# Kernel optimization log

Hardware: AMD Instinct MI355X
Metric: run time of the kernel (lower is better)

## Reference

```python
import jax, jax.numpy as jnp
import numpy as np

N_HEAD = 32
N_KV_HEAD = 8
HEAD_DIM = 64
N_EMBD = 2048
B, T = 2, 2048
ROPE_BASE = 10000.0


def _rope_cos_sin(T, head_dim, dtype):
    pos = jnp.arange(T, dtype=jnp.float32)
    dim_arr = jnp.arange(0, head_dim, 2, dtype=jnp.float32)
    freqs = ROPE_BASE ** (-dim_arr / head_dim)
    theta = jnp.outer(pos, freqs)                      # [T, hd/2]
    cos = jnp.concatenate([jnp.cos(theta), jnp.cos(theta)], axis=-1)  # [T, hd]
    sin = jnp.concatenate([jnp.sin(theta), jnp.sin(theta)], axis=-1)
    # broadcast to [1, T, 1, hd]
    return cos[None, :, None, :].astype(dtype), sin[None, :, None, :].astype(dtype)


def _rotate_half(v):
    h = v.shape[-1] // 2
    return jnp.concatenate([-v[..., h:], v[..., :h]], axis=-1)


def setup_inputs() -> dict:
    key = jax.random.key(0)
    kx, kq, kk, kv, ko = jax.random.split(key, 5)
    s = 1.0 / np.sqrt(N_EMBD)
    return {
        "x": jax.random.normal(kx, (B, T, N_EMBD), dtype=jnp.float32),
        "wq": jax.random.normal(kq, (N_EMBD, N_HEAD * HEAD_DIM), dtype=jnp.float32) * s,
        "wk": jax.random.normal(kk, (N_EMBD, N_KV_HEAD * HEAD_DIM), dtype=jnp.float32) * s,
        "wv": jax.random.normal(kv, (N_EMBD, N_KV_HEAD * HEAD_DIM), dtype=jnp.float32) * s,
        "wo": jax.random.normal(ko, (N_HEAD * HEAD_DIM, N_EMBD), dtype=jnp.float32) * s,
    }


def reference(x, wq, wk, wv, wo):
    Bx, Tx, C = x.shape
    n_rep = N_HEAD // N_KV_HEAD

    xq = (x @ wq).reshape(Bx, Tx, N_HEAD, HEAD_DIM)
    xk = (x @ wk).reshape(Bx, Tx, N_KV_HEAD, HEAD_DIM)
    xv = (x @ wv).reshape(Bx, Tx, N_KV_HEAD, HEAD_DIM)

    cos, sin = _rope_cos_sin(Tx, HEAD_DIM, x.dtype)
    xq = xq * cos + _rotate_half(xq) * sin
    xk = xk * cos + _rotate_half(xk) * sin

    # GQA: repeat_interleave KV heads to match query heads
    xk = jnp.repeat(xk, n_rep, axis=2)  # [B, T, H, hd]
    xv = jnp.repeat(xv, n_rep, axis=2)

    scale = 1.0 / np.sqrt(HEAD_DIM)
    # scores: [B, H, T, T]
    scores = jnp.einsum("bqhd,bkhd->bhqk", xq, xk) * scale
    causal = jnp.tril(jnp.ones((Tx, Tx), dtype=bool))
    scores = jnp.where(causal[None, None], scores, -jnp.inf)
    probs = jax.nn.softmax(scores, axis=-1)

    out = jnp.einsum("bhqk,bkhd->bqhd", probs, xv).reshape(Bx, Tx, N_HEAD * HEAD_DIM)
    return out @ wo
```

## Files before the change

kernel.cpp:

```cpp
#include <hip/hip_runtime.h>
#include <hip/hip_bf16.h>
#include <cstdint>
#include <cstddef>

#define B_ 2
#define T_ 2048
#define H_ 32
#define KVH_ 8
#define D_ 64
#define C_ 2048
#define NQKV 3072

typedef short short8 __attribute__((ext_vector_type(8)));
typedef float f32x4 __attribute__((ext_vector_type(4)));
typedef unsigned short u16;

__device__ __forceinline__ u16 f2b(float f) {
  union { float f; unsigned u; } x; x.f = f;
  unsigned r = x.u + 0x7fffu + ((x.u >> 16) & 1u);
  return (u16)(r >> 16);
}

__device__ __forceinline__ void gload16(const void* g, void* l) {
  __builtin_amdgcn_global_load_lds(
      (const __attribute__((address_space(1))) unsigned int*)g,
      (__attribute__((address_space(3))) unsigned int*)l,
      16, 0, 0);
}

__device__ __forceinline__ f32x4 mfma16(short8 a, short8 b, f32x4 c) {
  return __builtin_amdgcn_mfma_f32_16x16x32_bf16(a, b, c, 0, 0, 0);
}

__device__ __forceinline__ unsigned cvtpk(float lo_, float hi_) {
  unsigned r;
  asm("v_cvt_pk_bf16_f32 %0, %1, %2" : "=v"(r) : "v"(lo_), "v"(hi_));
  return r;
}

__global__ void k_tbl(float* __restrict__ tbl) {
  int i = blockIdx.x * 256 + threadIdx.x;
  int t = i >> 5, f = i & 31;
  double freq = pow(10000.0, -(double)f / 32.0);
  double th = (double)t * freq;
  tbl[i * 2 + 0] = (float)cos(th);
  tbl[i * 2 + 1] = (float)sin(th);
}

__global__ void k_cvtx(const float* __restrict__ x, u16* __restrict__ xb) {
  int i = blockIdx.x * 256 + threadIdx.x;
  float4 v = ((const float4*)x)[i];
  ushort4 o;
  o.x = f2b(v.x); o.y = f2b(v.y); o.z = f2b(v.z); o.w = f2b(v.w);
  ((ushort4*)xb)[i] = o;
}

__global__ void k_transw(const float* __restrict__ src, u16* __restrict__ dst, int N) {
  __shared__ float t[32][33];
  int tx = threadIdx.x, ty = threadIdx.y;
  int k0 = blockIdx.y * 32, n0 = blockIdx.x * 32;
#pragma unroll
  for (int i = 0; i < 4; i++)
    t[ty + i * 8][tx] = src[(size_t)(k0 + ty + i * 8) * N + n0 + tx];
  __syncthreads();
#pragma unroll
  for (int i = 0; i < 4; i++) {
    int nl = ty + i * 8;
    dst[(size_t)(n0 + nl) * 2048 + k0 + tx] = f2b(t[tx][nl]);
  }
}

__global__ __launch_bounds__(256, 2) void k_gemm(const u16* __restrict__ A,
                                                 const u16* __restrict__ Bt,
                                                 float* __restrict__ Cc,
                                                 int M, int N, int K) {
  __shared__ __align__(16) u16 As[128 * 32];
  __shared__ __align__(16) u16 Bs[128 * 32];
  const int tid = threadIdx.x;
  const int w = tid >> 6, l = tid & 63;
  const int lo = l & 15, hi = l >> 4;
  const int m0 = blockIdx.y * 128, n0 = blockIdx.x * 128;
  const int wr = w >> 1, wc = w & 1;
  f32x4 acc[4][4];
#pragma unroll
  for (int i = 0; i < 4; i++)
#pragma unroll
    for (int j = 0; j < 4; j++) acc[i][j] = (f32x4){0.f, 0.f, 0.f, 0.f};

  for (int k0 = 0; k0 < K; k0 += 32) {
#pragma unroll
    for (int i = 0; i < 2; i++) {
      int cid = i * 256 + tid;
      int row = cid >> 2, kc = cid & 3;
      gload16(A + (size_t)(m0 + row) * K + k0 + kc * 8, &As[(i * 256 + w * 64) * 8]);
      gload16(Bt + (size_t)(n0 + row) * K + k0 + kc * 8, &Bs[(i * 256 + w * 64) * 8]);
    }
    __syncthreads();
    short8 a[4], b[4];
#pragma unroll
    for (int i = 0; i < 4; i++)
      a[i] = *(const short8*)&As[(wr * 64 + i * 16 + lo) * 32 + hi * 8];
#pragma unroll
    for (int j = 0; j < 4; j++)
      b[j] = *(const short8*)&Bs[(wc * 64 + j * 16 + lo) * 32 + hi * 8];
#pragma unroll
    for (int i = 0; i < 4; i++)
#pragma unroll
      for (int j = 0; j < 4; j++) acc[i][j] = mfma16(a[i], b[j], acc[i][j]);
    __syncthreads();
  }
  const int r0 = m0 + wr * 64, c0 = n0 + wc * 64;
#pragma unroll
  for (int i = 0; i < 4; i++)
#pragma unroll
    for (int j = 0; j < 4; j++) {
      f32x4 v = acc[i][j];
      int col = c0 + j * 16 + lo;
      int rw = r0 + i * 16 + hi * 4;
#pragma unroll
      for (int r = 0; r < 4; r++) Cc[(size_t)(rw + r) * N + col] = v[r];
    }
}

__global__ void k_rope(const float* __restrict__ QKV, const float* __restrict__ tbl,
                       u16* __restrict__ Qb, u16* __restrict__ Kb, u16* __restrict__ Vb) {
  int bt = blockIdx.x;
  int b = bt >> 11, t = bt & 2047;
  const float* row = QKV + (size_t)bt * NQKV;
  const float2* cs = (const float2*)tbl + (size_t)t * 32;
  int tid = threadIdx.x;
  const float QS = 0.125f * 1.44269504089f;
#pragma unroll
  for (int i = 0; i < 4; i++) {
    int p = i * 256 + tid;
    int h = p >> 5, dd = p & 31;
    float2 c = cs[dd];
    float q0 = row[h * 64 + dd], q1 = row[h * 64 + dd + 32];
    float o0 = (q0 * c.x - q1 * c.y) * QS;
    float o1 = (q1 * c.x + q0 * c.y) * QS;
    size_t base = ((size_t)(b * H_ + h) * T_ + t) * 64 + dd;
    Qb[base] = f2b(o0);
    Qb[base + 32] = f2b(o1);
  }
  {
    int kvh = tid >> 5, dd = tid & 31;
    float2 c = cs[dd];
    float k0v = row[2048 + kvh * 64 + dd], k1v = row[2048 + kvh * 64 + dd + 32];
    size_t base = ((size_t)(b * KVH_ + kvh) * T_ + t) * 64 + dd;
    Kb[base] = f2b(k0v * c.x - k1v * c.y);
    Kb[base + 32] = f2b(k1v * c.x + k0v * c.y);
  }
#pragma unroll
  for (int i = 0; i < 2; i++) {
    int e = i * 256 + tid;
    int kvh = e >> 6, dd = e & 63;
    Vb[((size_t)(b * KVH_ + kvh) * T_ + t) * 64 + dd] = f2b(row[2560 + e]);
  }
}

__global__ void k_vtrans(const u16* __restrict__ Vb, u16* __restrict__ Vt) {
  __shared__ u16 tl[64][65];
  int bk = blockIdx.y;
  int t0 = blockIdx.x * 64;
  int tid = threadIdx.x;
#pragma unroll
  for (int i = 0; i < 16; i++) {
    int e = i * 256 + tid;
    int tlc = e >> 6, d = e & 63;
    tl[tlc][d] = Vb[((size_t)bk * T_ + t0 + tlc) * 64 + d];
  }
  __syncthreads();
#pragma unroll
  for (int i = 0; i < 16; i++) {
    int e = i * 256 + tid;
    int d = e >> 6, tc = e & 63;
    Vt[((size_t)bk * 64 + d) * T_ + t0 + tc] = tl[tc][d];
  }
}

#define PSTR 40
__global__ __launch_bounds__(256)
__attribute__((amdgpu_waves_per_eu(3, 3)))
void k_attn(const u16* __restrict__ Qb,
            const u16* __restrict__ Kb,
            const u16* __restrict__ Vt,
            u16* __restrict__ Ob) {
  __shared__ __align__(16) u16 Pl[4][2][16 * PSTR];
  const int tid = threadIdx.x, w = tid >> 6, l = tid & 63;
  const int lo = l & 15, hi = l >> 4;
  const int b = blockIdx.z, h = blockIdx.y, kvh = h >> 2;
  const int tile = (w < 2) ? (int)blockIdx.x : (31 - (int)blockIdx.x);
  const int q0 = tile * 64 + (w & 1) * 32;

  const size_t qbase = (size_t)(b * H_ + h) * T_ * 64;
  const size_t kbase = (size_t)(b * KVH_ + kvh) * T_ * 64;
  const size_t vbase = (size_t)(b * KVH_ + kvh) * 64 * T_;

  short8 aq[2][2];
#pragma unroll
  for (int qt = 0; qt < 2; qt++)
#pragma unroll
    for (int hf = 0; hf < 2; hf++)
      aq[qt][hf] = *(const short8*)&Qb[qbase + (size_t)(q0 + qt * 16 + lo) * 64 + hf * 32 + hi * 8];

  f32x4 o[2][4];
  float m[2], lsum[2];
#pragma unroll
  for (int qt = 0; qt < 2; qt++) {
    m[qt] = -1e30f; lsum[qt] = 0.f;
#pragma unroll
    for (int jd = 0; jd < 4; jd++) o[qt][jd] = (f32x4){0.f, 0.f, 0.f, 0.f};
  }

  auto LOADK = [&](short8 (&ak)[2][2], int kv0) {
#pragma unroll
    for (int f = 0; f < 2; f++)
#pragma unroll
      for (int hf = 0; hf < 2; hf++)
        ak[f][hf] = *(const short8*)&Kb[kbase + (size_t)(kv0 + f * 16 + lo) * 64 + hf * 32 + hi * 8];
  };

  auto STEP = [&](const short8 (&ak)[2][2], int kv0, bool masked) {
    short8 av[4];
#pragma unroll
    for (int jd = 0; jd < 4; jd++)
      av[jd] = *(const short8*)&Vt[vbase + (size_t)(jd * 16 + lo) * T_ + kv0 + hi * 8];

    f32x4 s[2][2];
    __builtin_amdgcn_s_setprio(1);
#pragma unroll
    for (int qt = 0; qt < 2; qt++)
#pragma unroll
      for (int f = 0; f < 2; f++) {
        f32x4 acc = (f32x4){0.f, 0.f, 0.f, 0.f};
        acc = mfma16(ak[f][0], aq[qt][0], acc);
        acc = mfma16(ak[f][1], aq[qt][1], acc);
        s[qt][f] = acc;
      }
    __builtin_amdgcn_s_setprio(0);

#pragma unroll
    for (int qt = 0; qt < 2; qt++) {
      const int myq = q0 + qt * 16 + lo;
      float p[8];
#pragma unroll
      for (int f = 0; f < 2; f++)
#pragma unroll
        for (int r = 0; r < 4; r++) {
          float v = s[qt][f][r];
          if (masked) {
            int kv = kv0 + f * 16 + hi * 4 + r;
            v = (kv <= myq) ? v : -1e30f;
          }
          p[f * 4 + r] = v;
        }
      float mx = fmaxf(fmaxf(fmaxf(p[0], p[1]), fmaxf(p[2], p[3])),
                       fmaxf(fmaxf(p[4], p[5]), fmaxf(p[6], p[7])));
      mx = fmaxf(mx, __shfl_xor(mx, 16));
      mx = fmaxf(mx, __shfl_xor(mx, 32));
      if (!__all(mx <= m[qt] + 11.5f)) {
        float mn = fmaxf(m[qt], mx);
        float a_ = exp2f(m[qt] - mn);
        m[qt] = mn;
        lsum[qt] *= a_;
#pragma unroll
        for (int jd = 0; jd < 4; jd++) {
          f32x4 t = o[qt][jd];
#pragma unroll
          for (int r = 0; r < 4; r++) t[r] *= a_;
          o[qt][jd] = t;
        }
      }
      float sm = 0.f;
#pragma unroll
      for (int i = 0; i < 8; i++) { p[i] = exp2f(p[i] - m[qt]); sm += p[i]; }
      sm += __shfl_xor(sm, 16);
      sm += __shfl_xor(sm, 32);
      lsum[qt] += sm;
      uint2 w0, w1;
      w0.x = cvtpk(p[0], p[1]); w0.y = cvtpk(p[2], p[3]);
      w1.x = cvtpk(p[4], p[5]); w1.y = cvtpk(p[6], p[7]);
      *(uint2*)&Pl[w][qt][lo * PSTR + hi * 4] = w0;
      *(uint2*)&Pl[w][qt][lo * PSTR + 16 + hi * 4] = w1;
    }

#pragma unroll
    for (int qt = 0; qt < 2; qt++) {
      short8 pb = *(const short8*)&Pl[w][qt][lo * PSTR + hi * 8];
      __builtin_amdgcn_s_setprio(1);
#pragma unroll
      for (int jd = 0; jd < 4; jd++) o[qt][jd] = mfma16(av[jd], pb, o[qt][jd]);
      __builtin_amdgcn_s_setprio(0);
    }
  };

  short8 akA[2][2], akB[2][2];
  LOADK(akA, 0);
  int kv0 = 0;
  while (kv0 + 64 <= q0) {
    LOADK(akB, kv0 + 32);
    STEP(akA, kv0, false);
    LOADK(akA, kv0 + 64);
    STEP(akB, kv0 + 32, false);
    kv0 += 64;
  }
  if (kv0 < q0) {
    LOADK(akB, q0);
    STEP(akA, kv0, false);
    STEP(akB, q0, true);
  } else {
    STEP(akA, q0, true);
  }

#pragma unroll
  for (int qt = 0; qt < 2; qt++) {
    const int myq = q0 + qt * 16 + lo;
    float inv = 1.0f / lsum[qt];
    size_t obase = ((size_t)(b * T_ + myq) * H_ + h) * 64;
#pragma unroll
    for (int jd = 0; jd < 4; jd++) {
      ushort4 ov;
      ov.x = f2b(o[qt][jd][0] * inv);
      ov.y = f2b(o[qt][jd][1] * inv);
      ov.z = f2b(o[qt][jd][2] * inv);
      ov.w = f2b(o[qt][jd][3] * inv);
      *(ushort4*)&Ob[obase + jd * 16 + hi * 4] = ov;
    }
  }
}

constexpr size_t OFF_TBL = 0;
constexpr size_t SZ_TBL = (size_t)T_ * 32 * 2 * 4;
constexpr size_t OFF_XB = OFF_TBL + SZ_TBL;
constexpr size_t SZ_XB = (size_t)B_ * T_ * C_ * 2;
constexpr size_t OFF_WQKVT = OFF_XB + SZ_XB;
constexpr size_t SZ_WQKVT = (size_t)NQKV * C_ * 2;
constexpr size_t OFF_WOT = OFF_WQKVT + SZ_WQKVT;
constexpr size_t SZ_WOT = (size_t)C_ * C_ * 2;
constexpr size_t OFF_QKV = OFF_WOT + SZ_WOT;
constexpr size_t SZ_QKV = (size_t)B_ * T_ * NQKV * 4;
constexpr size_t OFF_QB = OFF_QKV + SZ_QKV;
constexpr size_t SZ_QB = (size_t)B_ * H_ * T_ * D_ * 2;
constexpr size_t OFF_KB = OFF_QB + SZ_QB;
constexpr size_t SZ_KVB = (size_t)B_ * KVH_ * T_ * D_ * 2;
constexpr size_t OFF_VB = OFF_KB + SZ_KVB;
constexpr size_t OFF_VT = OFF_VB + SZ_KVB;
constexpr size_t OFF_OB = OFF_VT + SZ_KVB;
constexpr size_t SZ_OB = (size_t)B_ * T_ * H_ * D_ * 2;

extern "C" void kernel_launch(void* const* d_in, const int* in_sizes, int n_in,
                              void* d_out, int out_size, void* d_ws, size_t ws_size,
                              hipStream_t stream) {
  const float* x = (const float*)d_in[0];
  const float* wq = (const float*)d_in[1];
  const float* wk = (const float*)d_in[2];
  const float* wv = (const float*)d_in[3];
  const float* wo = (const float*)d_in[4];

  char* ws = (char*)d_ws;
  float* tbl = (float*)(ws + OFF_TBL);
  u16* xb = (u16*)(ws + OFF_XB);
  u16* wqkvT = (u16*)(ws + OFF_WQKVT);
  u16* woT = (u16*)(ws + OFF_WOT);
  float* qkv = (float*)(ws + OFF_QKV);
  u16* Qb = (u16*)(ws + OFF_QB);
  u16* Kb = (u16*)(ws + OFF_KB);
  u16* Vb = (u16*)(ws + OFF_VB);
  u16* Vt = (u16*)(ws + OFF_VT);
  u16* Ob = (u16*)(ws + OFF_OB);

  k_tbl<<<256, 256, 0, stream>>>(tbl);
  k_cvtx<<<8192, 256, 0, stream>>>(x, xb);
  dim3 tb(32, 8);
  k_transw<<<dim3(64, 64), tb, 0, stream>>>(wq, wqkvT, 2048);
  k_transw<<<dim3(16, 64), tb, 0, stream>>>(wk, wqkvT + (size_t)2048 * 2048, 512);
  k_transw<<<dim3(16, 64), tb, 0, stream>>>(wv, wqkvT + (size_t)2560 * 2048, 512);
  k_transw<<<dim3(64, 64), tb, 0, stream>>>(wo, woT, 2048);

  k_gemm<<<dim3(NQKV / 128, (B_ * T_) / 128), 256, 0, stream>>>(xb, wqkvT, qkv,
                                                                B_ * T_, NQKV, C_);
  k_rope<<<B_ * T_, 256, 0, stream>>>(qkv, tbl, Qb, Kb, Vb);
  k_vtrans<<<dim3(T_ / 64, B_ * KVH_), 256, 0, stream>>>(Vb, Vt);
  k_attn<<<dim3(16, H_, B_), 256, 0, stream>>>(Qb, Kb, Vt, Ob);
  k_gemm<<<dim3(C_ / 128, (B_ * T_) / 128), 256, 0, stream>>>(Ob, woT, (float*)d_out,
                                                              B_ * T_, C_, C_);
}
```

Measured before the change: 294.5 us.

## Use single-wave attention blocks and compute softmax row sums via MFMA

Reworks the attention kernel so that each block holds one 64-lane wave processing 32 query rows. Blocks are ordered longest-first in place of the paired causal-balanced 4-wave blocks, which gives the hardware scheduler finer-grained load balancing. The per-step softmax sum reduction (two cross-lane shuffles) is replaced by an extra MFMA that multiplies the probability tile by a ones vector. This accumulates row sums in matrix accumulators, adding one MFMA per query tile per step.

```diff
diff --git a/kernel.cpp b/kernel.cpp
--- a/kernel.cpp
+++ b/kernel.cpp
@@ -179,18 +179,18 @@
 }
 
 #define PSTR 40
-__global__ __launch_bounds__(256)
+__global__ __launch_bounds__(64)
 __attribute__((amdgpu_waves_per_eu(3, 3)))
 void k_attn(const u16* __restrict__ Qb,
             const u16* __restrict__ Kb,
             const u16* __restrict__ Vt,
             u16* __restrict__ Ob) {
-  __shared__ __align__(16) u16 Pl[4][2][16 * PSTR];
-  const int tid = threadIdx.x, w = tid >> 6, l = tid & 63;
+  __shared__ __align__(16) u16 Pl[2][16 * PSTR];
+  const int l = threadIdx.x & 63;
   const int lo = l & 15, hi = l >> 4;
   const int b = blockIdx.z, h = blockIdx.y, kvh = h >> 2;
-  const int tile = (w < 2) ? (int)blockIdx.x : (31 - (int)blockIdx.x);
-  const int q0 = tile * 64 + (w & 1) * 32;
+  const int tile = 63 - (int)blockIdx.x;
+  const int q0 = tile * 32;
 
   const size_t qbase = (size_t)(b * H_ + h) * T_ * 64;
   const size_t kbase = (size_t)(b * KVH_ + kvh) * T_ * 64;
@@ -203,11 +203,16 @@
     for (int hf = 0; hf < 2; hf++)
       aq[qt][hf] = *(const short8*)&Qb[qbase + (size_t)(q0 + qt * 16 + lo) * 64 + hf * 32 + hi * 8];
 
-  f32x4 o[2][4];
-  float m[2], lsum[2];
+  short8 ones;
+#pragma unroll
+  for (int i = 0; i < 8; i++) ones[i] = (short)0x3F80;
+
+  f32x4 o[2][4], ls[2];
+  float m[2];
 #pragma unroll
   for (int qt = 0; qt < 2; qt++) {
-    m[qt] = -1e30f; lsum[qt] = 0.f;
+    m[qt] = -1e30f;
+    ls[qt] = (f32x4){0.f, 0.f, 0.f, 0.f};
 #pragma unroll
     for (int jd = 0; jd < 4; jd++) o[qt][jd] = (f32x4){0.f, 0.f, 0.f, 0.f};
   }
@@ -262,7 +267,8 @@
         float mn = fmaxf(m[qt], mx);
         float a_ = exp2f(m[qt] - mn);
         m[qt] = mn;
-        lsum[qt] *= a_;
+#pragma unroll
+        for (int r = 0; r < 4; r++) ls[qt][r] *= a_;
 #pragma unroll
         for (int jd = 0; jd < 4; jd++) {
           f32x4 t = o[qt][jd];
@@ -271,25 +277,22 @@
           o[qt][jd] = t;
         }
       }
-      float sm = 0.f;
-#pragma unroll
-      for (int i = 0; i < 8; i++) { p[i] = exp2f(p[i] - m[qt]); sm += p[i]; }
-      sm += __shfl_xor(sm, 16);
-      sm += __shfl_xor(sm, 32);
-      lsum[qt] += sm;
+#pragma unroll
+      for (int i = 0; i < 8; i++) p[i] = exp2f(p[i] - m[qt]);
       uint2 w0, w1;
       w0.x = cvtpk(p[0], p[1]); w0.y = cvtpk(p[2], p[3]);
       w1.x = cvtpk(p[4], p[5]); w1.y = cvtpk(p[6], p[7]);
-      *(uint2*)&Pl[w][qt][lo * PSTR + hi * 4] = w0;
-      *(uint2*)&Pl[w][qt][lo * PSTR + 16 + hi * 4] = w1;
+      *(uint2*)&Pl[qt][lo * PSTR + hi * 4] = w0;
+      *(uint2*)&Pl[qt][lo * PSTR + 16 + hi * 4] = w1;
     }
 
 #pragma unroll
     for (int qt = 0; qt < 2; qt++) {
-      short8 pb = *(const short8*)&Pl[w][qt][lo * PSTR + hi * 8];
+      short8 pb = *(const short8*)&Pl[qt][lo * PSTR + hi * 8];
       __builtin_amdgcn_s_setprio(1);
 #pragma unroll
       for (int jd = 0; jd < 4; jd++) o[qt][jd] = mfma16(av[jd], pb, o[qt][jd]);
+      ls[qt] = mfma16(ones, pb, ls[qt]);
       __builtin_amdgcn_s_setprio(0);
     }
   };
@@ -315,7 +318,7 @@
 #pragma unroll
   for (int qt = 0; qt < 2; qt++) {
     const int myq = q0 + qt * 16 + lo;
-    float inv = 1.0f / lsum[qt];
+    float inv = 1.0f / ls[qt][0];
     size_t obase = ((size_t)(b * T_ + myq) * H_ + h) * 64;
 #pragma unroll
     for (int jd = 0; jd < 4; jd++) {
@@ -381,7 +384,7 @@
                                                                 B_ * T_, NQKV, C_);
   k_rope<<<B_ * T_, 256, 0, stream>>>(qkv, tbl, Qb, Kb, Vb);
   k_vtrans<<<dim3(T_ / 64, B_ * KVH_), 256, 0, stream>>>(Vb, Vt);
-  k_attn<<<dim3(16, H_, B_), 256, 0, stream>>>(Qb, Kb, Vt, Ob);
+  k_attn<<<dim3(64, H_, B_), 64, 0, stream>>>(Qb, Kb, Vt, Ob);
   k_gemm<<<dim3(C_ / 128, (B_ * T_) / 128), 256, 0, stream>>>(Ob, woT, (float*)d_out,
                                                               B_ * T_, C_, C_);
 }
```

Result: slower. 342.1 us (+16.1%).

## Store QKV projection in bf16 and pair attention tiles per wave

Applied to the files above, without the earlier changes.

The QKV GEMM now writes bf16 instead of fp32, roughly halving the intermediate traffic between it and the RoPE kernel, which now reads bf16 and passes V through without conversion. The attention kernel is restructured so each wave processes two 32-row query tiles in sequence (tile p and 63-p), balancing the causal workload within every wave. The grid is halved to 8 blocks in x. The extra bf16 rounding of Q/K/V before RoPE may change accuracy slightly, and the halved grid with two serial passes per wave lowers available parallelism.

```diff
diff --git a/kernel.cpp b/kernel.cpp
--- a/kernel.cpp
+++ b/kernel.cpp
@@ -21,6 +21,11 @@
   return (u16)(r >> 16);
 }
 
+__device__ __forceinline__ float b2f(u16 v) {
+  union { unsigned u; float f; } x; x.u = ((unsigned)v) << 16;
+  return x.f;
+}
+
 __device__ __forceinline__ void gload16(const void* g, void* l) {
   __builtin_amdgcn_global_load_lds(
       (const __attribute__((address_space(1))) unsigned int*)g,
@@ -70,9 +75,10 @@
   }
 }
 
+template <bool BF16OUT>
 __global__ __launch_bounds__(256, 2) void k_gemm(const u16* __restrict__ A,
                                                  const u16* __restrict__ Bt,
-                                                 float* __restrict__ Cc,
+                                                 void* __restrict__ Cc,
                                                  int M, int N, int K) {
   __shared__ __align__(16) u16 As[128 * 32];
   __shared__ __align__(16) u16 Bs[128 * 32];
@@ -118,15 +124,20 @@
       int col = c0 + j * 16 + lo;
       int rw = r0 + i * 16 + hi * 4;
 #pragma unroll
-      for (int r = 0; r < 4; r++) Cc[(size_t)(rw + r) * N + col] = v[r];
-    }
-}
-
-__global__ void k_rope(const float* __restrict__ QKV, const float* __restrict__ tbl,
+      for (int r = 0; r < 4; r++) {
+        if (BF16OUT)
+          ((u16*)Cc)[(size_t)(rw + r) * N + col] = f2b(v[r]);
+        else
+          ((float*)Cc)[(size_t)(rw + r) * N + col] = v[r];
+      }
+    }
+}
+
+__global__ void k_rope(const u16* __restrict__ QKV, const float* __restrict__ tbl,
                        u16* __restrict__ Qb, u16* __restrict__ Kb, u16* __restrict__ Vb) {
   int bt = blockIdx.x;
   int b = bt >> 11, t = bt & 2047;
-  const float* row = QKV + (size_t)bt * NQKV;
+  const u16* row = QKV + (size_t)bt * NQKV;
   const float2* cs = (const float2*)tbl + (size_t)t * 32;
   int tid = threadIdx.x;
   const float QS = 0.125f * 1.44269504089f;
@@ -135,7 +146,7 @@
     int p = i * 256 + tid;
     int h = p >> 5, dd = p & 31;
     float2 c = cs[dd];
-    float q0 = row[h * 64 + dd], q1 = row[h * 64 + dd + 32];
+    float q0 = b2f(row[h * 64 + dd]), q1 = b2f(row[h * 64 + dd + 32]);
     float o0 = (q0 * c.x - q1 * c.y) * QS;
     float o1 = (q1 * c.x + q0 * c.y) * QS;
     size_t base = ((size_t)(b * H_ + h) * T_ + t) * 64 + dd;
@@ -145,7 +156,7 @@
   {
     int kvh = tid >> 5, dd = tid & 31;
     float2 c = cs[dd];
-    float k0v = row[2048 + kvh * 64 + dd], k1v = row[2048 + kvh * 64 + dd + 32];
+    float k0v = b2f(row[2048 + kvh * 64 + dd]), k1v = b2f(row[2048 + kvh * 64 + dd + 32]);
     size_t base = ((size_t)(b * KVH_ + kvh) * T_ + t) * 64 + dd;
     Kb[base] = f2b(k0v * c.x - k1v * c.y);
     Kb[base + 32] = f2b(k1v * c.x + k0v * c.y);
@@ -154,7 +165,7 @@
   for (int i = 0; i < 2; i++) {
     int e = i * 256 + tid;
     int kvh = e >> 6, dd = e & 63;
-    Vb[((size_t)(b * KVH_ + kvh) * T_ + t) * 64 + dd] = f2b(row[2560 + e]);
+    Vb[((size_t)(b * KVH_ + kvh) * T_ + t) * 64 + dd] = row[2560 + e];
   }
 }
 
@@ -189,28 +200,13 @@
   const int tid = threadIdx.x, w = tid >> 6, l = tid & 63;
   const int lo = l & 15, hi = l >> 4;
   const int b = blockIdx.z, h = blockIdx.y, kvh = h >> 2;
-  const int tile = (w < 2) ? (int)blockIdx.x : (31 - (int)blockIdx.x);
-  const int q0 = tile * 64 + (w & 1) * 32;
+  const int p = (int)blockIdx.x * 4 + w;
 
   const size_t qbase = (size_t)(b * H_ + h) * T_ * 64;
   const size_t kbase = (size_t)(b * KVH_ + kvh) * T_ * 64;
   const size_t vbase = (size_t)(b * KVH_ + kvh) * 64 * T_;
 
-  short8 aq[2][2];
-#pragma unroll
-  for (int qt = 0; qt < 2; qt++)
-#pragma unroll
-    for (int hf = 0; hf < 2; hf++)
-      aq[qt][hf] = *(const short8*)&Qb[qbase + (size_t)(q0 + qt * 16 + lo) * 64 + hf * 32 + hi * 8];
-
-  f32x4 o[2][4];
-  float m[2], lsum[2];
-#pragma unroll
-  for (int qt = 0; qt < 2; qt++) {
-    m[qt] = -1e30f; lsum[qt] = 0.f;
-#pragma unroll
-    for (int jd = 0; jd < 4; jd++) o[qt][jd] = (f32x4){0.f, 0.f, 0.f, 0.f};
-  }
+  int q0;
 
   auto LOADK = [&](short8 (&ak)[2][2], int kv0) {
 #pragma unroll
@@ -220,111 +216,132 @@
         ak[f][hf] = *(const short8*)&Kb[kbase + (size_t)(kv0 + f * 16 + lo) * 64 + hf * 32 + hi * 8];
   };
 
-  auto STEP = [&](const short8 (&ak)[2][2], int kv0, bool masked) {
-    short8 av[4];
-#pragma unroll
-    for (int jd = 0; jd < 4; jd++)
-      av[jd] = *(const short8*)&Vt[vbase + (size_t)(jd * 16 + lo) * T_ + kv0 + hi * 8];
-
-    f32x4 s[2][2];
-    __builtin_amdgcn_s_setprio(1);
+  for (int pass = 0; pass < 2; pass++) {
+    const int tile = pass ? (63 - p) : p;
+    q0 = tile * 32;
+
+    short8 aq[2][2];
 #pragma unroll
     for (int qt = 0; qt < 2; qt++)
 #pragma unroll
-      for (int f = 0; f < 2; f++) {
-        f32x4 acc = (f32x4){0.f, 0.f, 0.f, 0.f};
-        acc = mfma16(ak[f][0], aq[qt][0], acc);
-        acc = mfma16(ak[f][1], aq[qt][1], acc);
-        s[qt][f] = acc;
+      for (int hf = 0; hf < 2; hf++)
+        aq[qt][hf] = *(const short8*)&Qb[qbase + (size_t)(q0 + qt * 16 + lo) * 64 + hf * 32 + hi * 8];
+
+    f32x4 o[2][4];
+    float m[2], lsum[2];
+#pragma unroll
+    for (int qt = 0; qt < 2; qt++) {
+      m[qt] = -1e30f; lsum[qt] = 0.f;
+#pragma unroll
+      for (int jd = 0; jd < 4; jd++) o[qt][jd] = (f32x4){0.f, 0.f, 0.f, 0.f};
+    }
+
+    auto STEP = [&](const short8 (&ak)[2][2], int kv0, bool masked) {
+      short8 av[4];
+#pragma unroll
+      for (int jd = 0; jd < 4; jd++)
+        av[jd] = *(const short8*)&Vt[vbase + (size_t)(jd * 16 + lo) * T_ + kv0 + hi * 8];
+
+      f32x4 s[2][2];
+      __builtin_amdgcn_s_setprio(1);
+#pragma unroll
+      for (int qt = 0; qt < 2; qt++)
+#pragma unroll
+        for (int f = 0; f < 2; f++) {
+          f32x4 acc = (f32x4){0.f, 0.f, 0.f, 0.f};
+          acc = mfma16(ak[f][0], aq[qt][0], acc);
+          acc = mfma16(ak[f][1], aq[qt][1], acc);
+          s[qt][f] = acc;
+        }
+      __builtin_amdgcn_s_setprio(0);
+
+#pragma unroll
+      for (int qt = 0; qt < 2; qt++) {
+        const int myq = q0 + qt * 16 + lo;
+        float p_[8];
+#pragma unroll
+        for (int f = 0; f < 2; f++)
+#pragma unroll
+          for (int r = 0; r < 4; r++) {
+            float v = s[qt][f][r];
+            if (masked) {
+              int kv = kv0 + f * 16 + hi * 4 + r;
+              v = (kv <= myq) ? v : -1e30f;
+            }
+            p_[f * 4 + r] = v;
+          }
+        float mx = fmaxf(fmaxf(fmaxf(p_[0], p_[1]), fmaxf(p_[2], p_[3])),
+                         fmaxf(fmaxf(p_[4], p_[5]), fmaxf(p_[6], p_[7])));
+        mx = fmaxf(mx, __shfl_xor(mx, 16));
+        mx = fmaxf(mx, __shfl_xor(mx, 32));
+        if (!__all(mx <= m[qt] + 11.5f)) {
+          float mn = fmaxf(m[qt], mx);
+          float a_ = exp2f(m[qt] - mn);
+          m[qt] = mn;
+          lsum[qt] *= a_;
+#pragma unroll
+          for (int jd = 0; jd < 4; jd++) {
+            f32x4 t = o[qt][jd];
+#pragma unroll
+            for (int r = 0; r < 4; r++) t[r] *= a_;
+            o[qt][jd] = t;
+          }
+        }
+        float sm = 0.f;
+#pragma unroll
+        for (int i = 0; i < 8; i++) { p_[i] = exp2f(p_[i] - m[qt]); sm += p_[i]; }
+        sm += __shfl_xor(sm, 16);
+        sm += __shfl_xor(sm, 32);
+        lsum[qt] += sm;
+        uint2 w0, w1;
+        w0.x = cvtpk(p_[0], p_[1]); w0.y = cvtpk(p_[2], p_[3]);
+        w1.x = cvtpk(p_[4], p_[5]); w1.y = cvtpk(p_[6], p_[7]);
+        *(uint2*)&Pl[w][qt][lo * PSTR + hi * 4] = w0;
+        *(uint2*)&Pl[w][qt][lo * PSTR + 16 + hi * 4] = w1;
       }
-    __builtin_amdgcn_s_setprio(0);
+
+#pragma unroll
+      for (int qt = 0; qt < 2; qt++) {
+        short8 pb = *(const short8*)&Pl[w][qt][lo * PSTR + hi * 8];
+        __builtin_amdgcn_s_setprio(1);
+#pragma unroll
+        for (int jd = 0; jd < 4; jd++) o[qt][jd] = mfma16(av[jd], pb, o[qt][jd]);
+        __builtin_amdgcn_s_setprio(0);
+      }
+    };
+
+    short8 akA[2][2], akB[2][2];
+    LOADK(akA, 0);
+    int kv0 = 0;
+    while (kv0 + 64 <= q0) {
+      LOADK(akB, kv0 + 32);
+      STEP(akA, kv0, false);
+      LOADK(akA, kv0 + 64);
+      STEP(akB, kv0 + 32, false);
+      kv0 += 64;
+    }
+    if (kv0 < q0) {
+      LOADK(akB, q0);
+      STEP(akA, kv0, false);
+      STEP(akB, q0, true);
+    } else {
+      STEP(akA, q0, true);
+    }
 
 #pragma unroll
     for (int qt = 0; qt < 2; qt++) {
       const int myq = q0 + qt * 16 + lo;
-      float p[8];
-#pragma unroll
-      for (int f = 0; f < 2; f++)
-#pragma unroll
-        for (int r = 0; r < 4; r++) {
-          float v = s[qt][f][r];
-          if (masked) {
-            int kv = kv0 + f * 16 + hi * 4 + r;
-            v = (kv <= myq) ? v : -1e30f;
-          }
-          p[f * 4 + r] = v;
-        }
-      float mx = fmaxf(fmaxf(fmaxf(p[0], p[1]), fmaxf(p[2], p[3])),
-                       fmaxf(fmaxf(p[4], p[5]), fmaxf(p[6], p[7])));
-      mx = fmaxf(mx, __shfl_xor(mx, 16));
-      mx = fmaxf(mx, __shfl_xor(mx, 32));
-      if (!__all(mx <= m[qt] + 11.5f)) {
-        float mn = fmaxf(m[qt], mx);
-        float a_ = exp2f(m[qt] - mn);
-        m[qt] = mn;
-        lsum[qt] *= a_;
-#pragma unroll
-        for (int jd = 0; jd < 4; jd++) {
-          f32x4 t = o[qt][jd];
-#pragma unroll
-          for (int r = 0; r < 4; r++) t[r] *= a_;
-          o[qt][jd] = t;
-        }
+      float inv = 1.0f / lsum[qt];
+      size_t obase = ((size_t)(b * T_ + myq) * H_ + h) * 64;
+#pragma unroll
+      for (int jd = 0; jd < 4; jd++) {
+        ushort4 ov;
+        ov.x = f2b(o[qt][jd][0] * inv);
+        ov.y = f2b(o[qt][jd][1] * inv);
+        ov.z = f2b(o[qt][jd][2] * inv);
+        ov.w = f2b(o[qt][jd][3] * inv);
+        *(ushort4*)&Ob[obase + jd * 16 + hi * 4] = ov;
       }
-      float sm = 0.f;
-#pragma unroll
-      for (int i = 0; i < 8; i++) { p[i] = exp2f(p[i] - m[qt]); sm += p[i]; }
-      sm += __shfl_xor(sm, 16);
-      sm += __shfl_xor(sm, 32);
-      lsum[qt] += sm;
-      uint2 w0, w1;
-      w0.x = cvtpk(p[0], p[1]); w0.y = cvtpk(p[2], p[3]);
-      w1.x = cvtpk(p[4], p[5]); w1.y = cvtpk(p[6], p[7]);
-      *(uint2*)&Pl[w][qt][lo * PSTR + hi * 4] = w0;
-      *(uint2*)&Pl[w][qt][lo * PSTR + 16 + hi * 4] = w1;
-    }
-
-#pragma unroll
-    for (int qt = 0; qt < 2; qt++) {
-      short8 pb = *(const short8*)&Pl[w][qt][lo * PSTR + hi * 8];
-      __builtin_amdgcn_s_setprio(1);
-#pragma unroll
-      for (int jd = 0; jd < 4; jd++) o[qt][jd] = mfma16(av[jd], pb, o[qt][jd]);
-      __builtin_amdgcn_s_setprio(0);
-    }
-  };
-
-  short8 akA[2][2], akB[2][2];
-  LOADK(akA, 0);
-  int kv0 = 0;
-  while (kv0 + 64 <= q0) {
-    LOADK(akB, kv0 + 32);
-    STEP(akA, kv0, false);
-    LOADK(akA, kv0 + 64);
-    STEP(akB, kv0 + 32, false);
-    kv0 += 64;
-  }
-  if (kv0 < q0) {
-    LOADK(akB, q0);
-    STEP(akA, kv0, false);
-    STEP(akB, q0, true);
-  } else {
-    STEP(akA, q0, true);
-  }
-
-#pragma unroll
-  for (int qt = 0; qt < 2; qt++) {
-    const int myq = q0 + qt * 16 + lo;
-    float inv = 1.0f / lsum[qt];
-    size_t obase = ((size_t)(b * T_ + myq) * H_ + h) * 64;
-#pragma unroll
-    for (int jd = 0; jd < 4; jd++) {
-      ushort4 ov;
-      ov.x = f2b(o[qt][jd][0] * inv);
-      ov.y = f2b(o[qt][jd][1] * inv);
-      ov.z = f2b(o[qt][jd][2] * inv);
-      ov.w = f2b(o[qt][jd][3] * inv);
-      *(ushort4*)&Ob[obase + jd * 16 + hi * 4] = ov;
     }
   }
 }
@@ -338,7 +355,7 @@
 constexpr size_t OFF_WOT = OFF_WQKVT + SZ_WQKVT;
 constexpr size_t SZ_WOT = (size_t)C_ * C_ * 2;
 constexpr size_t OFF_QKV = OFF_WOT + SZ_WOT;
-constexpr size_t SZ_QKV = (size_t)B_ * T_ * NQKV * 4;
+constexpr size_t SZ_QKV = (size_t)B_ * T_ * NQKV * 2;
 constexpr size_t OFF_QB = OFF_QKV + SZ_QKV;
 constexpr size_t SZ_QB = (size_t)B_ * H_ * T_ * D_ * 2;
 constexpr size_t OFF_KB = OFF_QB + SZ_QB;
@@ -362,7 +379,7 @@
   u16* xb = (u16*)(ws + OFF_XB);
   u16* wqkvT = (u16*)(ws + OFF_WQKVT);
   u16* woT = (u16*)(ws + OFF_WOT);
-  float* qkv = (float*)(ws + OFF_QKV);
+  u16* qkv = (u16*)(ws + OFF_QKV);
   u16* Qb = (u16*)(ws + OFF_QB);
   u16* Kb = (u16*)(ws + OFF_KB);
   u16* Vb = (u16*)(ws + OFF_VB);
@@ -377,11 +394,11 @@
   k_transw<<<dim3(16, 64), tb, 0, stream>>>(wv, wqkvT + (size_t)2560 * 2048, 512);
   k_transw<<<dim3(64, 64), tb, 0, stream>>>(wo, woT, 2048);
 
-  k_gemm<<<dim3(NQKV / 128, (B_ * T_) / 128), 256, 0, stream>>>(xb, wqkvT, qkv,
-                                                                B_ * T_, NQKV, C_);
+  k_gemm<true><<<dim3(NQKV / 128, (B_ * T_) / 128), 256, 0, stream>>>(
+      xb, wqkvT, qkv, B_ * T_, NQKV, C_);
   k_rope<<<B_ * T_, 256, 0, stream>>>(qkv, tbl, Qb, Kb, Vb);
   k_vtrans<<<dim3(T_ / 64, B_ * KVH_), 256, 0, stream>>>(Vb, Vt);
-  k_attn<<<dim3(16, H_, B_), 256, 0, stream>>>(Qb, Kb, Vt, Ob);
-  k_gemm<<<dim3(C_ / 128, (B_ * T_) / 128), 256, 0, stream>>>(Ob, woT, (float*)d_out,
-                                                              B_ * T_, C_, C_);
-}
+  k_attn<<<dim3(8, H_, B_), 256, 0, stream>>>(Qb, Kb, Vt, Ob);
+  k_gemm<false><<<dim3(C_ / 128, (B_ * T_) / 128), 256, 0, stream>>>(
+      Ob, woT, d_out, B_ * T_, C_, C_);
+}
```

Result: faster. 273.8 us (-7.0%).
